# Optimization experiments

Measured on AMD Instinct MI355X. Metric: run time of the kernel, lower is better.

## Reference

```python
import jax, jax.numpy as jnp
import numpy as np

# Dimensions: B jets, P max particles, C coords, F features, K neighbors,
# H hidden units, O MLP output dim. Edge feature dim E = 2*(C+F).
B, P, C, F, K, H, O = 256, 128, 2, 7, 16, 128, 256
E = 2 * (C + F)
BIG = 1e9  # distance assigned to invalid (padded) neighbors


def setup_inputs() -> dict:
    key = jax.random.key(0)
    k1, k2, k3, k4 = jax.random.split(key, 4)
    raw = jax.random.normal(k1, (B, P, C + F), dtype=jnp.float32)
    # per-jet particle counts in [K+2, P]; padding is contiguous at the end
    lengths = jax.random.randint(k2, (B,), K + 2, P + 1)
    mask = (jnp.arange(P)[None, :] < lengths[:, None]).astype(jnp.float32)  # [B,P]
    # zero out padded rows and append mask as the last column (as the layer expects)
    x = jnp.concatenate([raw * mask[..., None], mask[..., None]], axis=-1)  # [B,P,C+F+1]
    W1 = jax.random.normal(k3, (E, H), dtype=jnp.float32) * (1.0 / np.sqrt(E))
    b1 = jnp.zeros((H,), dtype=jnp.float32)
    W2 = jax.random.normal(k4, (H, O), dtype=jnp.float32) * (1.0 / np.sqrt(H))
    b2 = jnp.zeros((O,), dtype=jnp.float32)
    return {"x": x, "W1": W1, "b1": b1, "W2": W2, "b2": b2}


def reference(x, W1, b1, W2, b2):
    coords = x[..., :C]          # [B,P,C]
    feats = x[..., C:-1]         # [B,P,F]
    mask = x[..., -1]            # [B,P] 1=real particle, 0=padding
    valid = mask > 0

    # --- kNN on coordinates (masked, vectorized over jets) ---
    diff = coords[:, :, None, :] - coords[:, None, :, :]      # [B,P,P,C]
    # squared distance: same ordering as tf.norm, avoids sqrt-at-zero issues
    dist2 = jnp.sum(diff * diff, axis=-1)                      # [B,P,P]
    dist2 = jnp.where(valid[:, None, :], dist2, BIG)           # mask padded neighbors
    _, idx = jax.lax.top_k(-dist2, K + 1)                      # [B,P,K+1]
    idx = idx[..., 1:]                                         # drop self -> [B,P,K]

    # --- gather neighbor coords/features ---
    idx_flat = idx.reshape(B, P * K)
    nbr_c = jnp.take_along_axis(coords, idx_flat[..., None], axis=1).reshape(B, P, K, C)
    nbr_f = jnp.take_along_axis(feats, idx_flat[..., None], axis=1).reshape(B, P, K, F)
    ctr_c = jnp.broadcast_to(coords[:, :, None, :], (B, P, K, C))
    ctr_f = jnp.broadcast_to(feats[:, :, None, :], (B, P, K, F))

    # edge features: [coord_i, feat_i, coord_j - coord_i, feat_j - feat_i]
    edge = jnp.concatenate([ctr_c, ctr_f, nbr_c - ctr_c, nbr_f - ctr_f], axis=-1)  # [B,P,K,E]

    # --- MLP + mean aggregation over neighbors ---
    h = jax.nn.relu(edge @ W1 + b1)   # [B,P,K,H]
    h = jax.nn.relu(h @ W2 + b2)      # [B,P,K,O]
    avg = jnp.mean(h, axis=2)         # [B,P,O]

    # append mask column; zero out padded particles (matches _fix_number_of_particles)
    out = jnp.concatenate([avg, jnp.ones((B, P, 1), avg.dtype)], axis=-1) * mask[..., None]
    return out
```

## Files before the change

kernel.cpp:

```cpp
#include <hip/hip_runtime.h>

#define BB 256
#define PP 128
#define KK 16
#define HH 128
#define OO 256
#define EE 18
#define XCH 10
#define BIGD 1000000000.0f
#define GPT 4

typedef __bf16 bf16x8 __attribute__((ext_vector_type(8)));
typedef __bf16 bf16x4 __attribute__((ext_vector_type(4)));
typedef float  f32x4  __attribute__((ext_vector_type(4)));

__global__ __launch_bounds__(256) void pack_w_kernel(const float* __restrict__ W1,
                                                     const float* __restrict__ W2,
                                                     __bf16* __restrict__ W2p,
                                                     __bf16* __restrict__ W1p) {
    const int t = blockIdx.x * 256 + threadIdx.x;
    if (t < 32768) {
        const int j  = t & 7;
        const int l  = (t >> 3) & 63;
        const int ks = (t >> 9) & 3;
        const int ct = t >> 11;
        const int row = ks * 32 + ((l >> 4) * 8) + j;
        const int col = ct * 16 + (l & 15);
        W2p[t] = (__bf16)W2[row * OO + col];
    } else {
        const int t2 = t - 32768;
        const int j  = t2 & 7;
        const int l  = (t2 >> 3) & 63;
        const int nt = t2 >> 9;
        const int k  = ((l >> 4) * 8) + j;
        const int n  = nt * 16 + (l & 15);
        W1p[t2] = (k < EE) ? (__bf16)W1[k * HH + n] : (__bf16)0.0f;
    }
}

__global__ __launch_bounds__(256, 4) void mlp_kernel(const float* __restrict__ x,
                                                     const __bf16* __restrict__ W1p,
                                                     const float* __restrict__ b1,
                                                     const __bf16* __restrict__ W2p,
                                                     const float* __restrict__ b2,
                                                     float* __restrict__ out) {
    __shared__ __bf16 sh1A[16 * 64 * 8];
    __shared__ int    sknn[GPT][KK];

    const int tid = threadIdx.x;
    const int lane = tid & 63;
    const int w = tid >> 6;
    const int quad = lane >> 4;
    const int lcol = lane & 15;

    const int pbase = blockIdx.x * GPT;
    const int bidx = pbase >> 7;
    const int i0 = pbase & (PP - 1);
    const float* xb = x + (size_t)bidx * PP * XCH;
    float* outrow = out + (size_t)pbase * (OO + 1);

    const float mq = xb[(i0 + quad) * XCH + (XCH - 1)];
    const int i = i0 + w;

    if (__all(mq == 0.0f)) {
        for (int o = tid; o < GPT * (OO + 1); o += 256) outrow[o] = 0.0f;
        return;
    }

    bf16x8 wf[8];
#pragma unroll
    for (int nt = 0; nt < 8; ++nt)
        wf[nt] = *(const bf16x8*)&W1p[(size_t)((nt * 64 + lane) * 8)];

    const float* ci = xb + i * XCH;
    const float2 a01 = *(const float2*)(ci + 0);
    const float2 a23 = *(const float2*)(ci + 2);
    const float2 a45 = *(const float2*)(ci + 4);
    const float2 a67 = *(const float2*)(ci + 6);
    const float  a8  = ci[8];
    const float  mw  = ci[XCH - 1];

    if (mw != 0.0f) {
        const float cix = a01.x;
        const float ciy = a01.y;

        const int j0 = lane, j1 = lane + 64;
        float d0, d1;
        {
            const float2 c0 = *(const float2*)(xb + j0 * XCH);
            const float m0 = xb[j0 * XCH + (XCH - 1)];
            float dx = cix - c0.x, dy = ciy - c0.y;
            d0 = __fadd_rn(__fmul_rn(dx, dx), __fmul_rn(dy, dy));
            if (m0 <= 0.0f || j0 == i) d0 = BIGD;
        }
        {
            const float2 c1 = *(const float2*)(xb + j1 * XCH);
            const float m1 = xb[j1 * XCH + (XCH - 1)];
            float dx = cix - c1.x, dy = ciy - c1.y;
            d1 = __fadd_rn(__fmul_rn(dx, dx), __fmul_rn(dy, dy));
            if (m1 <= 0.0f || j1 == i) d1 = BIGD;
        }

        const unsigned d0b = __float_as_uint(d0);
        const unsigned d1b = __float_as_uint(d1);

        unsigned long long A0 = ~0ull, A1 = ~0ull, W0 = 0ull, W1 = 0ull;
        int need = KK;
        int asz = 2 * 64;

        auto step = [&](unsigned long long q0, unsigned long long q1) {
            const unsigned long long z0 = A0 & q0;
            const unsigned long long z1 = A1 & q1;
            const int c = __popcll(z0) + __popcll(z1);
            if (c == need) { W0 |= z0; W1 |= z1; A0 = A1 = 0ull; need = 0; }
            else if (c > need) { A0 = z0; A1 = z1; asz = c; }
            else { W0 |= z0; W1 |= z1; need -= c; A0 &= ~z0; A1 &= ~z1; asz -= c; }
        };

#pragma unroll 1
        for (int t = 14; t >= 0; --t) {
            const unsigned dg0 = (d0b >> (2 * t + 1)) & 3u;
            const unsigned dg1 = (d1b >> (2 * t + 1)) & 3u;
            const unsigned long long p0_0  = __ballot(dg0 == 0u);
            const unsigned long long p1_0  = __ballot(dg1 == 0u);
            const unsigned long long p0_01 = __ballot(dg0 <= 1u);
            const unsigned long long p1_01 = __ballot(dg1 <= 1u);
            const unsigned long long p0_02 = __ballot(dg0 <= 2u);
            const unsigned long long p1_02 = __ballot(dg1 <= 2u);
            const unsigned long long z0_0  = A0 & p0_0,  z1_0  = A1 & p1_0;
            const unsigned long long z0_01 = A0 & p0_01, z1_01 = A1 & p1_01;
            const unsigned long long z0_02 = A0 & p0_02, z1_02 = A1 & p1_02;
            const int c0  = __popcll(z0_0)  + __popcll(z1_0);
            const int c01 = __popcll(z0_01) + __popcll(z1_01);
            const int c02 = __popcll(z0_02) + __popcll(z1_02);
            if (c0 >= need) {
                A0 = z0_0; A1 = z1_0; asz = c0;
            } else if (c01 >= need) {
                W0 |= z0_0; W1 |= z1_0; need -= c0;
                A0 = z0_01 & ~p0_0; A1 = z1_01 & ~p1_0; asz = c01 - c0;
            } else if (c02 >= need) {
                W0 |= z0_01; W1 |= z1_01; need -= c01;
                A0 = z0_02 & ~p0_01; A1 = z1_02 & ~p1_01; asz = c02 - c01;
            } else {
                W0 |= z0_02; W1 |= z1_02; need -= c02;
                A0 &= ~p0_02; A1 &= ~p1_02; asz -= c02;
            }
            if (asz == need) { W0 |= A0; W1 |= A1; A0 = A1 = 0ull; need = 0; break; }
        }
        if (need) {
            const unsigned long long q0 = __ballot((d0b & 1u) == 0u);
            const unsigned long long q1 = __ballot((d1b & 1u) == 0u);
            step(q0, q1);
        }
        if (need) step(~0ull, 0ull);
        {
            const unsigned long long M5 = 0x00000000FFFFFFFFull;
            const unsigned long long M4 = 0x0000FFFF0000FFFFull;
            const unsigned long long M3 = 0x00FF00FF00FF00FFull;
            const unsigned long long M2 = 0x0F0F0F0F0F0F0F0Full;
            const unsigned long long M1 = 0x3333333333333333ull;
            const unsigned long long M0 = 0x5555555555555555ull;
            if (need) step(M5, M5);
            if (need) step(M4, M4);
            if (need) step(M3, M3);
            if (need) step(M2, M2);
            if (need) step(M1, M1);
            if (need) step(M0, M0);
        }
        W0 |= A0; W1 |= A1;

        unsigned int mb0 = __builtin_amdgcn_mbcnt_lo((unsigned)(W0 & 0xffffffffull), 0u);
        mb0 = __builtin_amdgcn_mbcnt_hi((unsigned)(W0 >> 32), mb0);
        unsigned int mb1 = __builtin_amdgcn_mbcnt_lo((unsigned)(W1 & 0xffffffffull), 0u);
        mb1 = __builtin_amdgcn_mbcnt_hi((unsigned)(W1 >> 32), mb1);
        const int base1 = __popcll(W0);

        if ((W0 >> lane) & 1ull) sknn[w][mb0] = j0;
        if ((W1 >> lane) & 1ull) sknn[w][base1 + mb1] = j1;
    } else {
        if (lane < KK) sknn[w][lane] = 0;
    }

    const int jn = sknn[w][lcol];
    const float* cj = xb + jn * XCH;
    const float2 n01 = *(const float2*)(cj + 0);
    const float2 n23 = *(const float2*)(cj + 2);
    const float2 n45 = *(const float2*)(cj + 4);
    const float2 n67 = *(const float2*)(cj + 6);
    const float  n8  = cj[8];

    float v[8];
#pragma unroll
    for (int e = 0; e < 8; ++e) v[e] = 0.0f;
    if (quad == 0) {
        v[0] = a01.x; v[1] = a01.y; v[2] = a23.x; v[3] = a23.y;
        v[4] = a45.x; v[5] = a45.y; v[6] = a67.x; v[7] = a67.y;
    } else if (quad == 1) {
        v[0] = a8;
        v[1] = n01.x - a01.x; v[2] = n01.y - a01.y;
        v[3] = n23.x - a23.x; v[4] = n23.y - a23.y;
        v[5] = n45.x - a45.x; v[6] = n45.y - a45.y;
        v[7] = n67.x - a67.x;
    } else if (quad == 2) {
        v[0] = n67.y - a67.y;
        v[1] = n8 - a8;
    }

    bf16x8 ef;
#pragma unroll
    for (int e = 0; e < 8; ++e) ef[e] = (__bf16)v[e];

    const f32x4 z4 = {0.0f, 0.0f, 0.0f, 0.0f};
    f32x4 h[8];
#pragma unroll
    for (int nt = 0; nt < 8; ++nt)
        h[nt] = __builtin_amdgcn_mfma_f32_16x16x32_bf16(wf[nt], ef, z4, 0, 0, 0);

#pragma unroll
    for (int nt = 0; nt < 8; ++nt) {
        const int ks = nt >> 1;
        const int lp = (((nt * 2 + (quad >> 1)) & 3) << 4) | lcol;
        const f32x4 b1v = *(const f32x4*)&b1[nt * 16 + quad * 4];
        bf16x4 hv;
#pragma unroll
        for (int r = 0; r < 4; ++r)
            hv[r] = (__bf16)fmaxf(h[nt][r] + b1v[r], 0.0f);
        *(bf16x4*)&sh1A[((ks * GPT + w) * 64 + lp) * 8 + (quad & 1) * 4] = hv;
    }
    __syncthreads();

    const float mscale = mq * (1.0f / KK);
#pragma unroll
    for (int ch = 0; ch < 2; ++ch) {
        f32x4 acc[GPT][2];
#pragma unroll
        for (int g = 0; g < GPT; ++g) { acc[g][0] = z4; acc[g][1] = z4; }

#pragma unroll
        for (int ks = 0; ks < 4; ++ks) {
            bf16x8 af[GPT], bfr[2];
#pragma unroll
            for (int g = 0; g < GPT; ++g)
                af[g] = *(const bf16x8*)&sh1A[((ks * GPT + g) * 64 + lane) * 8];
#pragma unroll
            for (int c = 0; c < 2; ++c) {
                const int ct = ch * 2 + c;
                bfr[c] = *(const bf16x8*)&W2p[(size_t)((((w * 4 + ct) * 4 + ks) * 64 + lane) * 8)];
            }
#pragma unroll
            for (int g = 0; g < GPT; ++g)
#pragma unroll
                for (int c = 0; c < 2; ++c)
                    acc[g][c] = __builtin_amdgcn_mfma_f32_16x16x32_bf16(
                        af[g], bfr[c], acc[g][c], 0, 0, 0);
        }

#pragma unroll
        for (int c = 0; c < 2; ++c) {
            const int ct = ch * 2 + c;
            const int col = w * 64 + ct * 16 + lcol;
            const float bc = b2[col];
            float val = 0.0f;
#pragma unroll
            for (int g = 0; g < GPT; ++g) {
                float s = 0.0f;
#pragma unroll
                for (int r = 0; r < 4; ++r) s += fmaxf(acc[g][c][r] + bc, 0.0f);
                s += __shfl_xor(s, 16, 64);
                s += __shfl_xor(s, 32, 64);
                if (quad == g) val = s;
            }
            outrow[(size_t)quad * (OO + 1) + col] = val * mscale;
        }
    }
    if (tid < GPT) outrow[(size_t)tid * (OO + 1) + OO] = xb[(i0 + tid) * XCH + (XCH - 1)];
}

extern "C" void kernel_launch(void* const* d_in, const int* in_sizes, int n_in,
                              void* d_out, int out_size, void* d_ws, size_t ws_size,
                              hipStream_t stream) {
    const float* x  = (const float*)d_in[0];
    const float* W1 = (const float*)d_in[1];
    const float* b1 = (const float*)d_in[2];
    const float* W2 = (const float*)d_in[3];
    const float* b2 = (const float*)d_in[4];
    float* out = (float*)d_out;

    __bf16* W2p = (__bf16*)d_ws;
    __bf16* W1p = (__bf16*)((char*)d_ws + 65536);

    pack_w_kernel<<<144, 256, 0, stream>>>(W1, W2, W2p, W1p);

    const int nblocks = (BB * PP) / GPT;
    mlp_kernel<<<nblocks, 256, 0, stream>>>(x, W1p, b1, W2p, b2, out);
}
```

Before: 125.6 us.

## Process eight particles per block with 512 threads, splitting W2 columns across eight waves

Each block now handles eight particles with eight waves instead of four. In the second layer each wave owns 32 output columns rather than 64, and it loops over two groups of four particles. This halves the W2 fragment traffic per particle and doubles the shared-memory hidden buffer. The risks are larger blocks that may lower occupancy, and more particles per block that may include fewer fully padded groups to skip early.

```diff
diff --git a/kernel.cpp b/kernel.cpp
--- a/kernel.cpp
+++ b/kernel.cpp
@@ -8,7 +8,8 @@
 #define EE 18
 #define XCH 10
 #define BIGD 1000000000.0f
-#define GPT 4
+#define GPT 8
+#define NBLK ((BB * PP) / GPT)
 
 typedef __bf16 bf16x8 __attribute__((ext_vector_type(8)));
 typedef __bf16 bf16x4 __attribute__((ext_vector_type(4)));
@@ -38,13 +39,13 @@
     }
 }
 
-__global__ __launch_bounds__(256, 4) void mlp_kernel(const float* __restrict__ x,
+__global__ __launch_bounds__(512, 4) void mlp_kernel(const float* __restrict__ x,
                                                      const __bf16* __restrict__ W1p,
                                                      const float* __restrict__ b1,
                                                      const __bf16* __restrict__ W2p,
                                                      const float* __restrict__ b2,
                                                      float* __restrict__ out) {
-    __shared__ __bf16 sh1A[16 * 64 * 8];
+    __shared__ __bf16 sh1A[32 * 64 * 8];
     __shared__ int    sknn[GPT][KK];
 
     const int tid = threadIdx.x;
@@ -59,11 +60,12 @@
     const float* xb = x + (size_t)bidx * PP * XCH;
     float* outrow = out + (size_t)pbase * (OO + 1);
 
-    const float mq = xb[(i0 + quad) * XCH + (XCH - 1)];
+    const float m_lo = xb[(i0 + quad) * XCH + (XCH - 1)];
+    const float m_hi = xb[(i0 + 4 + quad) * XCH + (XCH - 1)];
     const int i = i0 + w;
 
-    if (__all(mq == 0.0f)) {
-        for (int o = tid; o < GPT * (OO + 1); o += 256) outrow[o] = 0.0f;
+    if (__all((m_lo == 0.0f) & (m_hi == 0.0f))) {
+        for (int o = tid; o < GPT * (OO + 1); o += 512) outrow[o] = 0.0f;
         return;
     }
 
@@ -229,48 +231,46 @@
     }
     __syncthreads();
 
-    const float mscale = mq * (1.0f / KK);
-#pragma unroll
-    for (int ch = 0; ch < 2; ++ch) {
-        f32x4 acc[GPT][2];
-#pragma unroll
-        for (int g = 0; g < GPT; ++g) { acc[g][0] = z4; acc[g][1] = z4; }
+#pragma unroll
+    for (int gh = 0; gh < 2; ++gh) {
+        f32x4 acc[4][2];
+#pragma unroll
+        for (int gi = 0; gi < 4; ++gi) { acc[gi][0] = z4; acc[gi][1] = z4; }
 
 #pragma unroll
         for (int ks = 0; ks < 4; ++ks) {
-            bf16x8 af[GPT], bfr[2];
-#pragma unroll
-            for (int g = 0; g < GPT; ++g)
-                af[g] = *(const bf16x8*)&sh1A[((ks * GPT + g) * 64 + lane) * 8];
-#pragma unroll
-            for (int c = 0; c < 2; ++c) {
-                const int ct = ch * 2 + c;
-                bfr[c] = *(const bf16x8*)&W2p[(size_t)((((w * 4 + ct) * 4 + ks) * 64 + lane) * 8)];
-            }
-#pragma unroll
-            for (int g = 0; g < GPT; ++g)
+            bf16x8 af[4], bfr[2];
+#pragma unroll
+            for (int gi = 0; gi < 4; ++gi)
+                af[gi] = *(const bf16x8*)&sh1A[((ks * GPT + gh * 4 + gi) * 64 + lane) * 8];
+#pragma unroll
+            for (int c = 0; c < 2; ++c)
+                bfr[c] = *(const bf16x8*)&W2p[(size_t)((((w * 2 + c) * 4 + ks) * 64 + lane) * 8)];
+#pragma unroll
+            for (int gi = 0; gi < 4; ++gi)
 #pragma unroll
                 for (int c = 0; c < 2; ++c)
-                    acc[g][c] = __builtin_amdgcn_mfma_f32_16x16x32_bf16(
-                        af[g], bfr[c], acc[g][c], 0, 0, 0);
-        }
-
+                    acc[gi][c] = __builtin_amdgcn_mfma_f32_16x16x32_bf16(
+                        af[gi], bfr[c], acc[gi][c], 0, 0, 0);
+        }
+
+        const float mp = (gh == 0) ? m_lo : m_hi;
+        const float mscale = mp * (1.0f / KK);
 #pragma unroll
         for (int c = 0; c < 2; ++c) {
-            const int ct = ch * 2 + c;
-            const int col = w * 64 + ct * 16 + lcol;
+            const int col = w * 32 + c * 16 + lcol;
             const float bc = b2[col];
             float val = 0.0f;
 #pragma unroll
-            for (int g = 0; g < GPT; ++g) {
+            for (int gi = 0; gi < 4; ++gi) {
                 float s = 0.0f;
 #pragma unroll
-                for (int r = 0; r < 4; ++r) s += fmaxf(acc[g][c][r] + bc, 0.0f);
+                for (int r = 0; r < 4; ++r) s += fmaxf(acc[gi][c][r] + bc, 0.0f);
                 s += __shfl_xor(s, 16, 64);
                 s += __shfl_xor(s, 32, 64);
-                if (quad == g) val = s;
+                if (quad == gi) val = s;
             }
-            outrow[(size_t)quad * (OO + 1) + col] = val * mscale;
+            outrow[(size_t)(gh * 4 + quad) * (OO + 1) + col] = val * mscale;
         }
     }
     if (tid < GPT) outrow[(size_t)tid * (OO + 1) + OO] = xb[(i0 + tid) * XCH + (XCH - 1)];
@@ -291,6 +291,5 @@
 
     pack_w_kernel<<<144, 256, 0, stream>>>(W1, W2, W2p, W1p);
 
-    const int nblocks = (BB * PP) / GPT;
-    mlp_kernel<<<nblocks, 256, 0, stream>>>(x, W1p, b1, W2p, b2, out);
+    mlp_kernel<<<NBLK, 512, 0, stream>>>(x, W1p, b1, W2p, b2, out);
 }
```

Measured after the change: 134.7 us. 1.07x slower.
